# Performance work log

Measured on AMD Instinct MI355X. Metric: run time of the kernel, lower is better.

Reference implementation:

```python
import jax, jax.numpy as jnp
import numpy as np
import math

N_SCALES = 8
WAVELET_LEN = 64
MIN_SCALE, MAX_SCALE = 1.0, 64.0
BATCH, SEQ, FEAT = 16, 4096, 64


def _morlet_init():
    # Faithful to _initialize_mother_wavelets
    t = np.linspace(-4.0, 4.0, WAVELET_LEN, dtype=np.float32)
    w = np.zeros((N_SCALES, WAVELET_LEN), dtype=np.float32)
    for i in range(N_SCALES):
        omega = 2.0 + i * 0.5
        sigma = 1.0 + i * 0.1
        wav = np.exp(-t ** 2 / (2 * sigma ** 2)) * np.cos(omega * t)
        w[i] = wav / np.linalg.norm(wav)
    return jnp.asarray(w)


def setup_inputs() -> dict:
    key = jax.random.key(0)
    k1, _ = jax.random.split(key)
    signal = jax.random.normal(k1, (BATCH, SEQ, FEAT), dtype=jnp.float32)
    mother_wavelets = _morlet_init()
    scale_weights = jnp.ones((N_SCALES,), dtype=jnp.float32)
    return {"signal": signal, "mother_wavelets": mother_wavelets, "scale_weights": scale_weights}


def _scales():
    return np.logspace(math.log10(MIN_SCALE), math.log10(MAX_SCALE), N_SCALES)


def _dilate(wavelet, scale):
    # F.interpolate(mode='linear', align_corners=True) to length int(WAVELET_LEN*scale)
    L_out = int(WAVELET_LEN * scale)
    if L_out > 1:
        pos = jnp.arange(L_out, dtype=jnp.float32) * ((WAVELET_LEN - 1) / (L_out - 1))
    else:
        pos = jnp.zeros((1,), dtype=jnp.float32)
    grid = jnp.arange(WAVELET_LEN, dtype=jnp.float32)
    return jnp.interp(pos, grid, wavelet) / math.sqrt(scale)


def reference(signal, mother_wavelets, scale_weights):
    # signal: (B, S, F) -> coefficients: (B, n_scales, S, F)
    B, S, F = signal.shape
    sig = jnp.swapaxes(signal, 1, 2)  # (B, F, S): batch all FFTs over b,f per scale
    scales = _scales()
    coeffs = []
    for i in range(N_SCALES):
        s = float(scales[i])
        w = _dilate(mother_wavelets[i], s)  # (L_dil,)
        n = S + w.shape[0] - 1
        n_fft = 2 ** int(math.ceil(math.log2(n)))
        Sf = jnp.fft.rfft(sig, n=n_fft, axis=-1)
        Wf = jnp.fft.rfft(w, n=n_fft)
        conv = jnp.fft.irfft(Sf * Wf, n=n_fft, axis=-1)[..., :S]  # (B, F, S)
        coeffs.append(conv)
    C = jnp.stack(coeffs, axis=1)            # (B, n_scales, F, S)
    C = jnp.swapaxes(C, 2, 3)                # (B, n_scales, S, F)
    return C * scale_weights[None, :, None, None]
```

## Files before the change

kernel.cpp:

```cpp
#include <hip/hip_runtime.h>
#include <hip/hip_bf16.h>
#include <math.h>

typedef __attribute__((ext_vector_type(8))) short bf16x8;
typedef __attribute__((ext_vector_type(4))) float f32x4;

#define NSC    8
#define SLEN   4096
#define FEAT   64
#define NQ     264
#define ATAB_B (NQ * 8 * 1024)

constexpr int L_[NSC]    = {64, 115, 210, 380, 689, 1248, 2261, 4096};
constexpr int CACT_[NSC] = {3, 5, 8, 13, 23, 40, 72, 129};

struct WavP { float step[NSC]; float isq[NSC]; };

__global__ void k_build_atab(const float* __restrict__ mw, const float* __restrict__ sw,
                             __hip_bfloat16* __restrict__ at, WavP wp)
{
  int e = blockIdx.x * 256 + threadIdx.x;
  int j = e & 7, l = (e >> 3) & 63, s = (e >> 9) & 7, q = e >> 12;
  int k = 16 * q - 32 + (l & 15) - 8 * (l >> 4) - j;
  float val = 0.f;
  if (k >= 0 && k < L_[s]) {
    float pos = (float)k * wp.step[s];
    int ii = (int)pos;
    float r;
    if (ii >= 63) r = mw[s * 64 + 63];
    else {
      float a = mw[s * 64 + ii];
      r = fmaf(pos - (float)ii, mw[s * 64 + ii + 1] - a, a);
    }
    val = r * wp.isq[s] * sw[s];
  }
  at[e] = __float2bfloat16(val);
}

__global__ __launch_bounds__(256) void k_transpose(const float* __restrict__ sig,
                                                   __hip_bfloat16* __restrict__ sigT2)
{
  __shared__ float t[4096];
  const int tid = threadIdx.x;
  const float* sp = sig + (size_t)blockIdx.x * 4096;
  for (int idx = tid; idx < 4096; idx += 256) {
    int r = idx >> 6, f = idx & 63;
    t[(r << 6) + (f ^ ((r & 7) << 3))] = sp[idx];
  }
  __syncthreads();
  __hip_bfloat16* op = sigT2 + (size_t)blockIdx.x * 4096;
  for (int e = tid; e < 4096; e += 256) {
    int h = e >> 11, n = (e >> 9) & 3, l = (e >> 3) & 63, i = e & 7;
    int f = n * 16 + (l & 15);
    int r = h * 32 + (l >> 4) * 8 + i;
    op[e] = __float2bfloat16(t[(r << 6) + (f ^ ((r & 7) << 3))]);
  }
}

template<int SB>
__device__ __forceinline__ void loadA4(const char* aw, int c_old, bf16x8* A) {
  #pragma unroll
  for (int i = 0; i < 4; ++i)
    if (c_old <= CACT_[SB + i])
      A[i] = *(const bf16x8*)(aw + (size_t)c_old * 16384 + (SB + i) * 1024);
}

__device__ __forceinline__ void loadB4(const char* cb2, int c_old, bf16x8* B) {
  const char* p = cb2 - (size_t)c_old * 4096;
  #pragma unroll
  for (int n = 0; n < 4; ++n)
    B[n] = *(const bf16x8*)(p + n * 1024);
}

template<int SB>
__device__ __forceinline__ void stepMFMA(int c_old, const bf16x8* A, const bf16x8* B,
                                         f32x4 (*acc)[4]) {
  __builtin_amdgcn_s_setprio(1);
  #pragma unroll
  for (int i = 3; i >= 0; --i) {
    if (c_old <= CACT_[SB + i]) {
      acc[i][0] = __builtin_amdgcn_mfma_f32_16x16x32_bf16(A[i], B[0], acc[i][0], 0, 0, 0);
      acc[i][1] = __builtin_amdgcn_mfma_f32_16x16x32_bf16(A[i], B[1], acc[i][1], 0, 0, 0);
      acc[i][2] = __builtin_amdgcn_mfma_f32_16x16x32_bf16(A[i], B[2], acc[i][2], 0, 0, 0);
      acc[i][3] = __builtin_amdgcn_mfma_f32_16x16x32_bf16(A[i], B[3], acc[i][3], 0, 0, 0);
    }
  }
  __builtin_amdgcn_s_setprio(0);
}

template<int SB>
__device__ __forceinline__ void run_pass(const char* aw, const char* cb2, int nsteps,
                                         float* ob, int trow, int fl) {
  f32x4 acc[4][4];
  const f32x4 z = {0.f, 0.f, 0.f, 0.f};
  #pragma unroll
  for (int i = 0; i < 4; ++i)
    #pragma unroll
    for (int n = 0; n < 4; ++n) acc[i][n] = z;

  bf16x8 A0[4], A1[4], B0[4], B1[4];
  loadA4<SB>(aw, 0, A0);
  loadB4(cb2, 0, B0);

  for (int st = 0; st < nsteps; st += 2) {
    loadA4<SB>(aw, st + 1, A1);
    loadB4(cb2, st + 1, B1);
    stepMFMA<SB>(st, A0, B0, acc);
    loadA4<SB>(aw, st + 2, A0);
    loadB4(cb2, st + 2, B0);
    stepMFMA<SB>(st + 1, A1, B1, acc);
  }

  #pragma unroll
  for (int i = 0; i < 4; ++i) {
    float* os = ob + (size_t)(SB + i) * SLEN * FEAT;
    #pragma unroll
    for (int n = 0; n < 4; ++n)
      #pragma unroll
      for (int r = 0; r < 4; ++r)
        os[(size_t)(trow + r) * FEAT + n * 16 + fl] = acc[i][n][r];
  }
}

__global__ __launch_bounds__(256, 3) void k_wavelet_mfma(
    const __hip_bfloat16* __restrict__ sigT2,
    const __hip_bfloat16* __restrict__ atab,
    float* __restrict__ out)
{
  const int tid = threadIdx.x;
  const int bid = blockIdx.x;
  const int tt  = 63 - (bid >> 4);
  const int b   = bid & 15;
  const int t0  = tt * 64;
  const int tw  = tid >> 6;
  const int l   = tid & 63;
  const int fl  = tid & 15;
  const int g   = (tid >> 4) & 3;

  const int C = tt + 1;
  const char* aw  = (const char*)atab + tw * 8192 + (size_t)l * 16;
  const char* cb2 = (const char*)sigT2 + ((size_t)((b * 64 + tt) * 2 + 1)) * 4096
                    + (size_t)l * 16;

  float* ob = out + (size_t)b * NSC * SLEN * FEAT;
  const int trow = t0 + tw * 16 + g * 4;

  run_pass<4>(aw, cb2, 2 * C, ob, trow, fl);
  run_pass<0>(aw, cb2, min(2 * C, 14), ob, trow, fl);
}

extern "C" void kernel_launch(void* const* d_in, const int* in_sizes, int n_in,
                              void* d_out, int out_size, void* d_ws, size_t ws_size,
                              hipStream_t stream) {
  const float* sig = (const float*)d_in[0];
  const float* mw  = (const float*)d_in[1];
  const float* sw  = (const float*)d_in[2];
  float*       out = (float*)d_out;

  __hip_bfloat16* atab  = (__hip_bfloat16*)d_ws;
  __hip_bfloat16* sigT2 = (__hip_bfloat16*)((char*)d_ws + 0x240000);

  WavP wp;
  const double lg = log10(64.0), st = lg / 7.0;
  for (int i = 0; i < NSC; ++i) {
    double y = (i == 7) ? lg : (double)i * st;
    double s = pow(10.0, y);
    wp.step[i] = (float)(63.0 / (double)(L_[i] - 1));
    wp.isq[i]  = (float)(1.0 / sqrt(s));
  }

  k_build_atab<<<NQ * 16, 256, 0, stream>>>(mw, sw, atab, wp);
  k_transpose<<<1024, 256, 0, stream>>>(sig, sigT2);
  k_wavelet_mfma<<<1024, 256, 0, stream>>>(sigT2, atab, out);
}
```

Baseline: 90.07 us.

## Stage signal B tiles into LDS with async global_load_lds double buffering

Each wave used to fetch the same signal B fragments straight from global memory. Now the whole block cooperatively loads 4-step chunks of the signal into a double-buffered LDS area with global_load_lds, and each wave reads its B operands from LDS. This is meant to cut redundant global/L2 traffic, since all four waves share the same B data, and to overlap the next chunk's load with the current MFMAs. In exchange it adds 32KB of LDS per block, which may limit occupancy, plus a block-wide barrier every chunk.

```diff
diff --git a/kernel.cpp b/kernel.cpp
--- a/kernel.cpp
+++ b/kernel.cpp
@@ -65,13 +65,6 @@
       A[i] = *(const bf16x8*)(aw + (size_t)c_old * 16384 + (SB + i) * 1024);
 }
 
-__device__ __forceinline__ void loadB4(const char* cb2, int c_old, bf16x8* B) {
-  const char* p = cb2 - (size_t)c_old * 4096;
-  #pragma unroll
-  for (int n = 0; n < 4; ++n)
-    B[n] = *(const bf16x8*)(p + n * 1024);
-}
-
 template<int SB>
 __device__ __forceinline__ void stepMFMA(int c_old, const bf16x8* A, const bf16x8* B,
                                          f32x4 (*acc)[4]) {
@@ -89,8 +82,10 @@
 }
 
 template<int SB>
-__device__ __forceinline__ void run_pass(const char* aw, const char* cb2, int nsteps,
-                                         float* ob, int trow, int fl) {
+__device__ __forceinline__ void run_pass(const char* aw, const char* sgb,
+                                         short (*lbuf)[8192], int nsteps,
+                                         int tid, int l, float* ob, int trow, int fl)
+{
   f32x4 acc[4][4];
   const f32x4 z = {0.f, 0.f, 0.f, 0.f};
   #pragma unroll
@@ -98,17 +93,46 @@
     #pragma unroll
     for (int n = 0; n < 4; ++n) acc[i][n] = z;
 
-  bf16x8 A0[4], A1[4], B0[4], B1[4];
+  const int nsc = (nsteps + 3) >> 2;
+
+  auto stage = [&](int sc) {
+    const char* gp = sgb - (size_t)(2 * sc + 1) * 8192 + tid * 16;
+    char* lp = (char*)lbuf[sc & 1] + (tid >> 6) * 1024;
+    #pragma unroll
+    for (int it = 0; it < 4; ++it)
+      __builtin_amdgcn_global_load_lds(
+        (const __attribute__((address_space(1))) void*)(gp + it * 4096),
+        (__attribute__((address_space(3))) void*)(lp + it * 4096), 16, 0, 0);
+  };
+  auto ldB = [&](int sc, int st, bf16x8* B) {
+    const char* p = (const char*)lbuf[sc & 1] + (3 - (st & 3)) * 4096 + l * 16;
+    #pragma unroll
+    for (int n = 0; n < 4; ++n)
+      B[n] = *(const bf16x8*)(p + n * 1024);
+  };
+
+  bf16x8 A0[4], A1[4], Ra[4], Rb[4];
+  stage(0);
   loadA4<SB>(aw, 0, A0);
-  loadB4(cb2, 0, B0);
-
-  for (int st = 0; st < nsteps; st += 2) {
-    loadA4<SB>(aw, st + 1, A1);
-    loadB4(cb2, st + 1, B1);
-    stepMFMA<SB>(st, A0, B0, acc);
+  loadA4<SB>(aw, 1, A1);
+  __syncthreads();
+
+  for (int sc = 0; sc < nsc; ++sc) {
+    const int st = 4 * sc;
+    if (sc + 1 < nsc) stage(sc + 1);
+    ldB(sc, st, Ra);
+    if (st + 1 < nsteps) ldB(sc, st + 1, Rb);
+    stepMFMA<SB>(st, A0, Ra, acc);
     loadA4<SB>(aw, st + 2, A0);
-    loadB4(cb2, st + 2, B0);
-    stepMFMA<SB>(st + 1, A1, B1, acc);
+    if (st + 2 < nsteps) ldB(sc, st + 2, Ra);
+    if (st + 1 < nsteps) stepMFMA<SB>(st + 1, A1, Rb, acc);
+    loadA4<SB>(aw, st + 3, A1);
+    if (st + 3 < nsteps) ldB(sc, st + 3, Rb);
+    if (st + 2 < nsteps) stepMFMA<SB>(st + 2, A0, Ra, acc);
+    loadA4<SB>(aw, st + 4, A0);
+    if (st + 3 < nsteps) stepMFMA<SB>(st + 3, A1, Rb, acc);
+    loadA4<SB>(aw, st + 5, A1);
+    __syncthreads();
   }
 
   #pragma unroll
@@ -127,6 +151,8 @@
     const __hip_bfloat16* __restrict__ atab,
     float* __restrict__ out)
 {
+  __shared__ __align__(16) short lbuf[2][8192];
+
   const int tid = threadIdx.x;
   const int bid = blockIdx.x;
   const int tt  = 63 - (bid >> 4);
@@ -139,14 +165,13 @@
 
   const int C = tt + 1;
   const char* aw  = (const char*)atab + tw * 8192 + (size_t)l * 16;
-  const char* cb2 = (const char*)sigT2 + ((size_t)((b * 64 + tt) * 2 + 1)) * 4096
-                    + (size_t)l * 16;
+  const char* sgb = (const char*)sigT2 + (size_t)(b * 64 + tt) * 8192;
 
   float* ob = out + (size_t)b * NSC * SLEN * FEAT;
   const int trow = t0 + tw * 16 + g * 4;
 
-  run_pass<4>(aw, cb2, 2 * C, ob, trow, fl);
-  run_pass<0>(aw, cb2, min(2 * C, 14), ob, trow, fl);
+  run_pass<4>(aw, sgb, lbuf, 2 * C, tid, l, ob, trow, fl);
+  run_pass<0>(aw, sgb, lbuf, min(2 * C, 14), tid, l, ob, trow, fl);
 }
 
 extern "C" void kernel_launch(void* const* d_in, const int* in_sizes, int n_in,
```

Result: faster. 86.52 us (-3.9%).
